# Optimization experiments

Hardware: AMD Instinct MI355X
Metric: run time of the kernel (lower is better)

The kernel has to match this reference:

```python
import jax, jax.numpy as jnp
import numpy as np

N_CHARS = 50257
CHAR = 512
HID = 1024
LENGTH = 2048


def setup_inputs() -> dict:
    key = jax.random.key(0)
    ks = jax.random.split(key, 8)
    s = 1.0 / np.sqrt(HID)
    sh = 1.0 / np.sqrt(HID)
    return {
        "inputs": jax.random.normal(ks[0], (HID,), jnp.float32),
        "embed": (jax.random.normal(ks[1], (N_CHARS, CHAR), jnp.float32) * 0.02),
        "W_ih": jax.random.uniform(ks[2], (4 * HID, CHAR), jnp.float32, -s, s),
        "W_hh": jax.random.uniform(ks[3], (4 * HID, HID), jnp.float32, -s, s),
        "b_ih": jax.random.uniform(ks[4], (4 * HID,), jnp.float32, -s, s),
        "b_hh": jax.random.uniform(ks[5], (4 * HID,), jnp.float32, -s, s),
        "W_head": jax.random.uniform(ks[6], (N_CHARS, HID), jnp.float32, -sh, sh),
        "b_head": jax.random.uniform(ks[7], (N_CHARS,), jnp.float32, -sh, sh),
        "length": LENGTH,
        "start": 5,
    }


def _lstm_cell(x, h, c, W_ih, W_hh, b_ih, b_hh):
    # PyTorch gate order: i, f, g, o
    gates = W_ih @ x + b_ih + W_hh @ h + b_hh  # [4H]
    i, f, g, o = jnp.split(gates, 4)
    i = jax.nn.sigmoid(i)
    f = jax.nn.sigmoid(f)
    g = jnp.tanh(g)
    o = jax.nn.sigmoid(o)
    c = f * c + i * g
    h = o * jnp.tanh(c)
    return h, c


def reference(inputs, embed, W_ih, W_hh, b_ih, b_hh, W_head, b_head, length, start):
    h0 = inputs                       # latent used as initial hidden state
    c0 = jnp.zeros_like(inputs)
    x0 = embed[start]                 # [CHAR]

    def step(carry, _):
        h, c, x = carry
        h, c = _lstm_cell(x, h, c, W_ih, W_hh, b_ih, b_hh)
        logits = W_head @ h + b_head  # [N_CHARS]
        char = jnp.argmax(logits)
        x = embed[char]
        return (h, c, x), (char, logits)

    _, (chars, logits) = jax.lax.scan(step, (h0, c0, x0), None, length=length)
    return chars, logits
```

## Files before the change

### kernel.cpp

```cpp
#include <hip/hip_runtime.h>
#include <stdint.h>
#include <math.h>

#define HID   1024
#define CHARD 512
#define NC    50257
#define TLEN  2048
#define NBLK  256
#define NTHR  512
#define NGRP2 2048
#define GR    25
#define GRREG 6
#define GRLDS 19
#define NBH   1571
#define SQ    4064.0f
#define INVSQ (1.0f/4064.0f)
#define QERR  (0.5f/4064.0f)
#define CANDR 192
#define FLAGSTRIDE 16

typedef unsigned long long ull;
typedef unsigned char u8;
typedef float f32x4 __attribute__((ext_vector_type(4)));

__device__ __forceinline__ unsigned ford(float f) {
    unsigned b = __float_as_uint(f);
    return (b & 0x80000000u) ? ~b : (b | 0x80000000u);
}
__device__ __forceinline__ float unford(unsigned u) {
    return __uint_as_float((u & 0x80000000u) ? (u & 0x7FFFFFFFu) : ~u);
}
__device__ __forceinline__ ull packkv(float v, unsigned j) {
    return ((ull)ford(v) << 32) | (ull)(0xFFFFFFFFu - j);
}
__device__ __forceinline__ unsigned ceil16(float v) {
    unsigned u = ford(v);
    return (u >> 16) + ((u & 0xFFFFu) ? 1u : 0u);
}
__device__ __forceinline__ ull umaxu(ull a, ull b) { return a > b ? a : b; }
__device__ __forceinline__ ull shflx_ull(ull v, int m) {
    unsigned lo = (unsigned)v, hi = (unsigned)(v >> 32);
    lo = __shfl_xor(lo, m);
    hi = __shfl_xor(hi, m);
    return ((ull)hi << 32) | lo;
}

#define ALOADF(p)    __hip_atomic_load((p), __ATOMIC_RELAXED, __HIP_MEMORY_SCOPE_AGENT)
#define ASTORE(p, v) __hip_atomic_store((p), (v), __ATOMIC_RELAXED, __HIP_MEMORY_SCOPE_AGENT)

__global__ __launch_bounds__(256) void k_init(const float* __restrict__ inputs,
                                              float* __restrict__ hh,
                                              float* __restrict__ c,
                                              unsigned* __restrict__ flagarea,
                                              unsigned* __restrict__ bm4,
                                              unsigned* __restrict__ abuf16)
{
    int g = blockIdx.x * 256 + threadIdx.x;
    if (g < HID) { hh[g] = inputs[g]; c[g] = 0.f; }
    for (int i = g; i < 2 * NBLK * FLAGSTRIDE; i += 2048) flagarea[i] = 0u;
    if (g < NGRP2) bm4[g] = 0u;
    for (int i = g; i < NC; i += 2048) abuf16[i] = 0u;
}

__global__ __launch_bounds__(256) void k_quant(const float* __restrict__ W,
                                               u8* __restrict__ W8)
{
    size_t base = ((size_t)blockIdx.x * 256 + threadIdx.x) * 16;
    if (base >= (size_t)NC * HID) return;
    const float4* src = (const float4*)(W + base);
    uint out[4];
    #pragma unroll
    for (int g = 0; g < 4; ++g) {
        float4 w = src[g];
        int a0 = (__float2int_rn(w.x * SQ) + 128) & 255;
        int a1 = (__float2int_rn(w.y * SQ) + 128) & 255;
        int a2 = (__float2int_rn(w.z * SQ) + 128) & 255;
        int a3 = (__float2int_rn(w.w * SQ) + 128) & 255;
        out[g] = (uint)(a0 | (a1 << 8) | (a2 << 16) | (a3 << 24));
    }
    *(uint4*)(W8 + base) = make_uint4(out[0], out[1], out[2], out[3]);
}

__device__ __forceinline__ float exact_logit(const float4* hs4,
                                             const float* __restrict__ W_head,
                                             const float* __restrict__ b_head,
                                             int j, int lane)
{
    const float4* wr = (const float4*)(W_head + (size_t)j * HID);
    float a = 0.f;
    #pragma unroll
    for (int m = 0; m < 4; ++m) {
        float4 w = wr[m * 64 + lane], v = hs4[m * 64 + lane];
        a = fmaf(w.x, v.x, a); a = fmaf(w.y, v.y, a);
        a = fmaf(w.z, v.z, a); a = fmaf(w.w, v.w, a);
    }
    #pragma unroll
    for (int off = 32; off > 0; off >>= 1) a += __shfl_xor(a, off);
    return a + b_head[j];
}

__device__ unsigned resolve_slim(const float4* hs4,
                                 const unsigned* bm4, const unsigned* abuf16,
                                 const float* __restrict__ W_head,
                                 const float* __restrict__ b_head,
                                 float Sh, unsigned gen16, int tid)
{
    __shared__ int s_cnt, s_gcnt;
    __shared__ int s_grps[32];
    __shared__ int s_rows[CANDR];
    __shared__ unsigned mred[8];
    __shared__ ull red8[8];

    const int wave = tid >> 6;
    const int lane = tid & 63;

    unsigned bv[4];
    unsigned m16 = 0u;
    #pragma unroll
    for (int k = 0; k < 4; ++k) {
        bv[k] = ALOADF(&bm4[tid * 4 + k]);
        if ((bv[k] & 0xFFFFu) == gen16) {
            unsigned v = bv[k] >> 16;
            if (v > m16) m16 = v;
        }
    }
    if (tid == 0) { s_cnt = 0; s_gcnt = 0; }
    #pragma unroll
    for (int off = 32; off > 0; off >>= 1) {
        unsigned o = __shfl_xor(m16, off);
        if (o > m16) m16 = o;
    }
    if (lane == 0) mred[wave] = m16;
    __syncthreads();
    m16 = mred[0];
    #pragma unroll
    for (int w = 1; w < 8; ++w) if (mred[w] > m16) m16 = mred[w];

    const float mtil_f = unford((m16 > 0 ? m16 - 1 : 0) << 16);
    const float E = QERR * Sh * 1.02f + 1e-4f;
    const float thresh = mtil_f - 2.0f * E;
    const unsigned th16 = ford(thresh) >> 16;

    #pragma unroll
    for (int k = 0; k < 4; ++k) {
        unsigned v = bv[k];
        if ((v & 0xFFFFu) == gen16 && (v >> 16) >= th16) {
            int p = atomicAdd(&s_gcnt, 1);
            if (p < 32) s_grps[p] = tid * 4 + k;
        }
    }
    __syncthreads();
    const int ngr = s_gcnt;
    int ncr;
    if (ngr <= 32) {
        for (int gq = wave; gq < ngr; gq += 8) {
            if (lane < GR) {
                const int j = s_grps[gq] * GR + lane;
                if (j < NC) {
                    unsigned a = ALOADF(&abuf16[j]);
                    if ((a & 0xFFFFu) == gen16 && (a >> 16) >= th16) {
                        int p = atomicAdd(&s_cnt, 1);
                        if (p < CANDR) s_rows[p] = j;
                    }
                }
            }
        }
        __syncthreads();
        ncr = s_cnt;
    } else ncr = CANDR + 1;

    ull best = 0ull;
    if (ncr <= CANDR) {
        for (int q = wave; q < ncr; q += 8) {
            const int j = s_rows[q];
            best = umaxu(best, packkv(exact_logit(hs4, W_head, b_head, j, lane),
                                      (unsigned)j));
        }
    } else {
        for (int i = wave; i < NGRP2; i += 8) {
            unsigned v = ALOADF(&bm4[i]);
            if ((v & 0xFFFFu) == gen16 && (v >> 16) >= th16) {
                const int j0 = i * GR;
                bool c = false;
                if (lane < GR && j0 + lane < NC) {
                    unsigned a = ALOADF(&abuf16[j0 + lane]);
                    c = ((a & 0xFFFFu) == gen16 && (a >> 16) >= th16);
                }
                ull cnd = __ballot(c);
                while (cnd) {
                    const int s = __builtin_ctzll(cnd);
                    cnd &= cnd - 1;
                    const int j = j0 + s;
                    best = umaxu(best, packkv(exact_logit(hs4, W_head, b_head, j, lane),
                                              (unsigned)j));
                }
            }
        }
    }
    __syncthreads();
    if (lane == 0) red8[wave] = best;
    __syncthreads();
    best = red8[0];
    #pragma unroll
    for (int w = 1; w < 8; ++w) best = umaxu(best, red8[w]);
    unsigned idx = 0xFFFFFFFFu - (unsigned)(best & 0xFFFFFFFFull);
    return idx < NC ? idx : (NC - 1);
}

__device__ __forceinline__ float dot16u(uint4 q, float4 h0, float4 h1,
                                        float4 h2, float4 h3)
{
    float a = 0.f;
    a = fmaf((float)(q.x & 255u), h0.x, a);
    a = fmaf((float)((q.x >> 8) & 255u), h0.y, a);
    a = fmaf((float)((q.x >> 16) & 255u), h0.z, a);
    a = fmaf((float)(q.x >> 24), h0.w, a);
    a = fmaf((float)(q.y & 255u), h1.x, a);
    a = fmaf((float)((q.y >> 8) & 255u), h1.y, a);
    a = fmaf((float)((q.y >> 16) & 255u), h1.z, a);
    a = fmaf((float)(q.y >> 24), h1.w, a);
    a = fmaf((float)(q.z & 255u), h2.x, a);
    a = fmaf((float)((q.z >> 8) & 255u), h2.y, a);
    a = fmaf((float)((q.z >> 16) & 255u), h2.z, a);
    a = fmaf((float)(q.z >> 24), h2.w, a);
    a = fmaf((float)(q.w & 255u), h3.x, a);
    a = fmaf((float)((q.w >> 8) & 255u), h3.y, a);
    a = fmaf((float)((q.w >> 16) & 255u), h3.z, a);
    a = fmaf((float)(q.w >> 24), h3.w, a);
    return a;
}

__global__ __launch_bounds__(NTHR, 1) void k_persist(
    const float* __restrict__ W_ih, const float* __restrict__ W_hh,
    const float* __restrict__ b_ih, const float* __restrict__ b_hh,
    const float* __restrict__ embed,
    const float* __restrict__ W_head, const float* __restrict__ b_head,
    const u8* __restrict__ W8,
    float* hh, unsigned* abuf16, unsigned* bm4,
    float* __restrict__ chars_out, const int* __restrict__ startp,
    unsigned* flags, unsigned* gen)
{
    __shared__ uint4  w8L[8][GRLDS][64];
    __shared__ float4 hs4[HID / 4];
    __shared__ float4 xs4[CHARD / 4];
    __shared__ float  sred[8], sred2[8];

    const int b    = blockIdx.x;
    const int tid  = threadIdx.x;
    const int wave = tid >> 6;
    const int lane = tid & 63;
    const int rL   = b * 4 + wave;
    const int g    = b * 8 + wave;
    const int jb   = g * GR;
    const u8* Wp   = W8 + (size_t)jb * HID;

    uint4 qb[GRREG];
    #pragma unroll
    for (int rr = 0; rr < GRREG; ++rr) {
        const int j = jb + rr;
        qb[rr] = (j < NC) ? ((const uint4*)(Wp + (size_t)rr * HID))[lane]
                          : make_uint4(0, 0, 0, 0);
    }
    #pragma unroll
    for (int rr = 0; rr < GRLDS; ++rr) {
        const int j = jb + GRREG + rr;
        w8L[wave][rr][lane] = (j < NC)
            ? ((const uint4*)(Wp + (size_t)(GRREG + rr) * HID))[lane]
            : make_uint4(0, 0, 0, 0);
    }

    float bsum[4] = {0.f, 0.f, 0.f, 0.f};
    if (wave < 4) {
        #pragma unroll
        for (int q = 0; q < 4; ++q) bsum[q] = b_ih[q * HID + rL] + b_hh[q * HID + rL];
    }
    float creg = 0.f;
    __syncthreads();

    float Sh;
    {
        float sa = 0.f;
        if (tid < 256) {
            float4 hv = ((const float4*)hh)[tid];
            hs4[tid] = hv;
            sa = fabsf(hv.x) + fabsf(hv.y) + fabsf(hv.z) + fabsf(hv.w);
        }
        #pragma unroll
        for (int off = 32; off > 0; off >>= 1) sa += __shfl_xor(sa, off);
        if (lane == 0) sred[wave] = sa;
        __syncthreads();
        Sh = 0.f;
        #pragma unroll
        for (int w = 0; w < 8; ++w) Sh += sred[w];
    }

    unsigned bk = 0;

    #define GRIDBAR()                                                              \
    do {                                                                           \
        ++bk;                                                                      \
        __syncthreads();                                                           \
        if (b == 0) {                                                              \
            if (tid > 0 && tid < NBLK) {                                           \
                int guard = 0;                                                     \
                while (ALOADF(&flags[tid * FLAGSTRIDE]) < bk) {                    \
                    __builtin_amdgcn_s_sleep(1);                                   \
                    if (++guard > (1 << 24)) break;                                \
                }                                                                  \
            }                                                                      \
            __syncthreads();                                                       \
            if (tid < NBLK)                                                        \
                ASTORE(&gen[tid * FLAGSTRIDE], bk);                                \
        } else {                                                                   \
            if (tid == 0) {                                                        \
                ASTORE(&flags[b * FLAGSTRIDE], bk);                                \
                int guard = 0;                                                     \
                while (ALOADF(&gen[b * FLAGSTRIDE]) < bk) {                        \
                    __builtin_amdgcn_s_sleep(1);                                   \
                    if (++guard > (1 << 24)) break;                                \
                }                                                                  \
            }                                                                      \
            __syncthreads();                                                       \
        }                                                                          \
    } while (0)

    for (int t = 0; t < TLEN; ++t) {
        unsigned idx;
        if (t == 0) {
            idx = (unsigned)startp[0];
        } else {
            idx = resolve_slim(hs4, bm4, abuf16, W_head, b_head, Sh,
                               (unsigned)t & 0xFFFFu, tid);
            if (b == 0 && tid == 0) chars_out[t - 1] = (float)idx;
        }
        if (tid < 128) xs4[tid] = ((const float4*)(embed + (size_t)idx * CHARD))[tid];
        __syncthreads();

        if (wave < 4) {
            float acc[4];
            #pragma unroll
            for (int q = 0; q < 4; ++q) {
                const float4* wi = (const float4*)(W_ih + (size_t)(q * HID + rL) * CHARD);
                const float4* wh = (const float4*)(W_hh + (size_t)(q * HID + rL) * HID);
                float a = 0.f;
                #pragma unroll
                for (int m = 0; m < 2; ++m) {
                    float4 w = wi[m * 64 + lane], v = xs4[m * 64 + lane];
                    a = fmaf(w.x, v.x, a); a = fmaf(w.y, v.y, a);
                    a = fmaf(w.z, v.z, a); a = fmaf(w.w, v.w, a);
                }
                #pragma unroll
                for (int m = 0; m < 4; ++m) {
                    float4 w = wh[m * 64 + lane], v = hs4[m * 64 + lane];
                    a = fmaf(w.x, v.x, a); a = fmaf(w.y, v.y, a);
                    a = fmaf(w.z, v.z, a); a = fmaf(w.w, v.w, a);
                }
                acc[q] = a;
            }
            #pragma unroll
            for (int q = 0; q < 4; ++q) {
                #pragma unroll
                for (int off = 32; off > 0; off >>= 1) acc[q] += __shfl_xor(acc[q], off);
            }
            if (lane == 0) {
                float ig = 1.f / (1.f + expf(-(acc[0] + bsum[0])));
                float fg = 1.f / (1.f + expf(-(acc[1] + bsum[1])));
                float gg = tanhf(acc[2] + bsum[2]);
                float og = 1.f / (1.f + expf(-(acc[3] + bsum[3])));
                creg = fg * creg + ig * gg;
                ASTORE(&hh[(size_t)(t + 1) * HID + rL], og * tanhf(creg));
            }
        }

        GRIDBAR();

        {
            float sa = 0.f, ss = 0.f;
            if (tid < 256) {
                float4 hv = ((const float4*)(hh + (size_t)(t + 1) * HID))[tid];
                hs4[tid] = hv;
                sa = fabsf(hv.x) + fabsf(hv.y) + fabsf(hv.z) + fabsf(hv.w);
                ss = hv.x + hv.y + hv.z + hv.w;
            }
            #pragma unroll
            for (int off = 32; off > 0; off >>= 1) {
                sa += __shfl_xor(sa, off);
                ss += __shfl_xor(ss, off);
            }
            if (lane == 0) { sred[wave] = sa; sred2[wave] = ss; }
        }
        __syncthreads();
        float Hsum = 0.f;
        Sh = 0.f;
        #pragma unroll
        for (int w = 0; w < 8; ++w) { Sh += sred[w]; Hsum += sred2[w]; }

        const float4 H0 = hs4[lane * 4 + 0];
        const float4 H1 = hs4[lane * 4 + 1];
        const float4 H2 = hs4[lane * 4 + 2];
        const float4 H3 = hs4[lane * 4 + 3];
        const unsigned genN = (unsigned)(t + 1) & 0xFFFFu;

        if (jb < NC) {
            ull pmw = 0ull;
            float sv = -3.0e38f;
            #pragma unroll
            for (int rr = 0; rr < GRREG; ++rr) {
                const int j = jb + rr;
                if (j < NC) {
                    float a = dot16u(qb[rr], H0, H1, H2, H3);
                    #pragma unroll
                    for (int off = 32; off > 0; off >>= 1) a += __shfl_xor(a, off);
                    const float v = (a - 128.f * Hsum) * INVSQ + b_head[j];
                    if (lane == rr) sv = v;
                    pmw = umaxu(pmw, packkv(v, (unsigned)j));
                }
            }
            #pragma unroll
            for (int rr = 0; rr < GRLDS; ++rr) {
                const int j = jb + GRREG + rr;
                if (j < NC) {
                    float a = dot16u(w8L[wave][rr][lane], H0, H1, H2, H3);
                    #pragma unroll
                    for (int off = 32; off > 0; off >>= 1) a += __shfl_xor(a, off);
                    const float v = (a - 128.f * Hsum) * INVSQ + b_head[j];
                    if (lane == GRREG + rr) sv = v;
                    pmw = umaxu(pmw, packkv(v, (unsigned)j));
                }
            }
            const float gtop = unford((unsigned)(pmw >> 32));
            const float E2 = QERR * Sh * 1.02f + 1e-4f;
            if (lane < GR && (jb + lane) < NC && sv >= gtop - 2.0f * E2)
                ASTORE(&abuf16[jb + lane], (ceil16(sv) << 16) | genN);
            if (lane == 0)
                ASTORE(&bm4[g], (ceil16(gtop) << 16) | genN);
        }

        GRIDBAR();
    }

    if (b == 0) {
        unsigned idx = resolve_slim(hs4, bm4, abuf16, W_head, b_head, Sh,
                                    (unsigned)TLEN & 0xFFFFu, tid);
        if (tid == 0) chars_out[TLEN - 1] = (float)idx;
    }
    #undef GRIDBAR
}

#define GJ 64
#define GT 128
#define GK 16
__global__ __launch_bounds__(256) void k_gemm(const float* __restrict__ W_head,
                                              const float* __restrict__ b_head,
                                              const float* __restrict__ hh,
                                              float* __restrict__ logits)
{
    __shared__ float Ws[GK][GJ + 4];
    __shared__ float Hs[GK][GT + 1];

    const int tid = threadIdx.x;
    const int j0 = blockIdx.x * GJ;
    const int t0 = blockIdx.y * GT;
    const int tj = tid & 15;
    const int tt = tid >> 4;

    const int wlj = tid >> 2;
    const int wlk = (tid & 3) * 4;
    const int hlt = tid >> 1;
    const int hlk = (tid & 1) * 8;
    const float* Wrow = W_head + (size_t)(j0 + wlj) * HID;
    const bool wvalid = (j0 + wlj) < NC;

    float acc[8][4];
    #pragma unroll
    for (int bb = 0; bb < 8; ++bb)
        #pragma unroll
        for (int a = 0; a < 4; ++a) acc[bb][a] = 0.f;

    for (int k0 = 0; k0 < HID; k0 += GK) {
        __syncthreads();
        float4 wv = wvalid ? *(const float4*)(Wrow + k0 + wlk) : make_float4(0, 0, 0, 0);
        Ws[wlk + 0][wlj] = wv.x; Ws[wlk + 1][wlj] = wv.y;
        Ws[wlk + 2][wlj] = wv.z; Ws[wlk + 3][wlj] = wv.w;
        const float* hp = hh + (size_t)(t0 + hlt + 1) * HID + k0 + hlk;
        float4 a0 = *(const float4*)hp;
        float4 a1 = *(const float4*)(hp + 4);
        Hs[hlk + 0][hlt] = a0.x; Hs[hlk + 1][hlt] = a0.y;
        Hs[hlk + 2][hlt] = a0.z; Hs[hlk + 3][hlt] = a0.w;
        Hs[hlk + 4][hlt] = a1.x; Hs[hlk + 5][hlt] = a1.y;
        Hs[hlk + 6][hlt] = a1.z; Hs[hlk + 7][hlt] = a1.w;
        __syncthreads();
        #pragma unroll
        for (int kk = 0; kk < GK; ++kk) {
            float4 w4 = *(const float4*)&Ws[kk][tj * 4];
            float hvv[8];
            #pragma unroll
            for (int bb = 0; bb < 8; ++bb) hvv[bb] = Hs[kk][tt + 16 * bb];
            #pragma unroll
            for (int bb = 0; bb < 8; ++bb) {
                acc[bb][0] = fmaf(w4.x, hvv[bb], acc[bb][0]);
                acc[bb][1] = fmaf(w4.y, hvv[bb], acc[bb][1]);
                acc[bb][2] = fmaf(w4.z, hvv[bb], acc[bb][2]);
                acc[bb][3] = fmaf(w4.w, hvv[bb], acc[bb][3]);
            }
        }
    }

    const int j = j0 + tj * 4;
    float b0 = (j + 0 < NC) ? b_head[j + 0] : 0.f;
    float b1 = (j + 1 < NC) ? b_head[j + 1] : 0.f;
    float b2 = (j + 2 < NC) ? b_head[j + 2] : 0.f;
    float b3 = (j + 3 < NC) ? b_head[j + 3] : 0.f;
    #pragma unroll
    for (int bb = 0; bb < 8; ++bb) {
        const int t = t0 + tt + 16 * bb;
        float* dst = logits + (size_t)t * NC + j;
        if (j + 3 < NC) {
            f32x4 o = { acc[bb][0] + b0, acc[bb][1] + b1,
                        acc[bb][2] + b2, acc[bb][3] + b3 };
            __builtin_nontemporal_store(o, (f32x4*)dst);
        } else {
            if (j + 0 < NC) dst[0] = acc[bb][0] + b0;
            if (j + 1 < NC) dst[1] = acc[bb][1] + b1;
            if (j + 2 < NC) dst[2] = acc[bb][2] + b2;
        }
    }
}

__global__ __launch_bounds__(256) void k_init_fb(const float* __restrict__ inputs,
                                                 const int* __restrict__ startp,
                                                 float* __restrict__ h0,
                                                 float* __restrict__ c,
                                                 ull* __restrict__ blockmax)
{
    int tid = blockIdx.x * 256 + threadIdx.x;
    if (tid < NBH) blockmax[tid] = (tid == 0) ? packkv(3.0e38f, (unsigned)startp[0]) : 0ull;
    if (tid < HID) { h0[tid] = inputs[tid]; c[tid] = 0.f; }
}

__global__ __launch_bounds__(256) void k_lstm_fb(const float* __restrict__ W_ih,
                                                 const float* __restrict__ W_hh,
                                                 const float* __restrict__ b_ih,
                                                 const float* __restrict__ b_hh,
                                                 const float* __restrict__ embed,
                                                 const ull* __restrict__ blockmax,
                                                 const float* __restrict__ h_in,
                                                 float* __restrict__ h_out,
                                                 float* __restrict__ c,
                                                 float* __restrict__ chars_out,
                                                 int t)
{
    __shared__ float4 xs4[CHARD / 4];
    __shared__ float4 hs4[HID / 4];
    __shared__ ull    red[256];
    const int tid = threadIdx.x;
    ull pm = 0ull;
    for (int i = tid; i < NBH; i += 256) pm = umaxu(pm, blockmax[i]);
    red[tid] = pm;
    __syncthreads();
    for (int s = 128; s > 0; s >>= 1) {
        if (tid < s) red[tid] = umaxu(red[tid], red[tid + s]);
        __syncthreads();
    }
    const unsigned idx = 0xFFFFFFFFu - (unsigned)(red[0] & 0xFFFFFFFFull);
    if (t > 0 && blockIdx.x == 0 && tid == 0) chars_out[t - 1] = (float)idx;
    const float4* ex = (const float4*)(embed + (size_t)idx * CHARD);
    if (tid < 128) xs4[tid] = ex[tid];
    hs4[tid] = ((const float4*)h_in)[tid];
    __syncthreads();
    const int wave = tid >> 6, lane = tid & 63;
    const int r = blockIdx.x * 4 + wave;
    float acc[4];
    #pragma unroll
    for (int q = 0; q < 4; ++q) {
        const float4* wi = (const float4*)(W_ih + (size_t)(q * HID + r) * CHARD);
        const float4* wh = (const float4*)(W_hh + (size_t)(q * HID + r) * HID);
        float a = 0.f;
        #pragma unroll
        for (int m = 0; m < 2; ++m) {
            float4 w = wi[m * 64 + lane], v = xs4[m * 64 + lane];
            a = fmaf(w.x, v.x, a); a = fmaf(w.y, v.y, a);
            a = fmaf(w.z, v.z, a); a = fmaf(w.w, v.w, a);
        }
        #pragma unroll
        for (int m = 0; m < 4; ++m) {
            float4 w = wh[m * 64 + lane], v = hs4[m * 64 + lane];
            a = fmaf(w.x, v.x, a); a = fmaf(w.y, v.y, a);
            a = fmaf(w.z, v.z, a); a = fmaf(w.w, v.w, a);
        }
        acc[q] = a;
    }
    #pragma unroll
    for (int q = 0; q < 4; ++q)
        #pragma unroll
        for (int off = 32; off > 0; off >>= 1) acc[q] += __shfl_xor(acc[q], off);
    if (lane == 0) {
        float zi = acc[0] + b_ih[r]           + b_hh[r];
        float zf = acc[1] + b_ih[HID + r]     + b_hh[HID + r];
        float zg = acc[2] + b_ih[2 * HID + r] + b_hh[2 * HID + r];
        float zo = acc[3] + b_ih[3 * HID + r] + b_hh[3 * HID + r];
        float ig = 1.f / (1.f + expf(-zi));
        float fg = 1.f / (1.f + expf(-zf));
        float gg = tanhf(zg);
        float og = 1.f / (1.f + expf(-zo));
        float cn = fg * c[r] + ig * gg;
        c[r] = cn;
        h_out[r] = og * tanhf(cn);
    }
}

__global__ __launch_bounds__(256) void k_head_fb(const float* __restrict__ W_head,
                                                 const float* __restrict__ b_head,
                                                 const float* __restrict__ h_in,
                                                 float* __restrict__ logits,
                                                 ull* __restrict__ blockmax)
{
    __shared__ float4 hs4[HID / 4];
    __shared__ ull    wmax[4];
    const int tid = threadIdx.x;
    hs4[tid] = ((const float4*)h_in)[tid];
    __syncthreads();
    const int wave = tid >> 6, lane = tid & 63;
    const int base = blockIdx.x * 32 + wave * 8;
    ull pm = 0ull;
    #pragma unroll
    for (int rep = 0; rep < 8; ++rep) {
        const int j = base + rep;
        if (j < NC) {
            const float4* w = (const float4*)(W_head + (size_t)j * HID);
            float a = 0.f;
            #pragma unroll
            for (int m = 0; m < 4; ++m) {
                float4 ww = w[m * 64 + lane], v = hs4[m * 64 + lane];
                a = fmaf(ww.x, v.x, a); a = fmaf(ww.y, v.y, a);
                a = fmaf(ww.z, v.z, a); a = fmaf(ww.w, v.w, a);
            }
            #pragma unroll
            for (int off = 32; off > 0; off >>= 1) a += __shfl_xor(a, off);
            const float v = a + b_head[j];
            if (lane == 0) __builtin_nontemporal_store(v, &logits[j]);
            pm = umaxu(pm, packkv(v, (unsigned)j));
        }
    }
    if (lane == 0) wmax[wave] = pm;
    __syncthreads();
    if (tid == 0)
        blockmax[blockIdx.x] = umaxu(umaxu(wmax[0], wmax[1]), umaxu(wmax[2], wmax[3]));
}

__global__ __launch_bounds__(256) void k_final_fb(const ull* __restrict__ blockmax,
                                                  float* __restrict__ chars_out)
{
    __shared__ ull red[256];
    const int tid = threadIdx.x;
    ull pm = 0ull;
    for (int i = tid; i < NBH; i += 256) pm = umaxu(pm, blockmax[i]);
    red[tid] = pm;
    __syncthreads();
    for (int s = 128; s > 0; s >>= 1) {
        if (tid < s) red[tid] = umaxu(red[tid], red[tid + s]);
        __syncthreads();
    }
    if (tid == 0)
        chars_out[TLEN - 1] = (float)(0xFFFFFFFFu - (unsigned)(red[0] & 0xFFFFFFFFull));
}

extern "C" void kernel_launch(void* const* d_in, const int* in_sizes, int n_in,
                              void* d_out, int out_size, void* d_ws, size_t ws_size,
                              hipStream_t stream)
{
    const float* inputs = (const float*)d_in[0];
    const float* embed  = (const float*)d_in[1];
    const float* W_ih   = (const float*)d_in[2];
    const float* W_hh   = (const float*)d_in[3];
    const float* b_ih   = (const float*)d_in[4];
    const float* b_hh   = (const float*)d_in[5];
    const float* W_head = (const float*)d_in[6];
    const float* b_head = (const float*)d_in[7];
    const int*   startp = (const int*)d_in[9];

    float* out        = (float*)d_out;
    float* chars_out  = out;
    float* logits_out = out + TLEN;

    char* ws = (char*)d_ws;
    const size_t off_hh  = 0;
    const size_t off_c   = off_hh + (size_t)(TLEN + 1) * HID * 4;
    const size_t off_ab  = (off_c + (size_t)HID * 4 + 15) & ~(size_t)15;
    const size_t off_bm  = (off_ab + (size_t)NC * 4 + 15) & ~(size_t)15;
    const size_t off_fl  = (off_bm + (size_t)NGRP2 * 4 + 63) & ~(size_t)63;
    const size_t off_w8  = (off_fl + (size_t)(2 * NBLK * FLAGSTRIDE) * 4 + 15)
                           & ~(size_t)15;
    const size_t need    = off_w8 + (size_t)NC * HID;

    if (ws_size >= need) {
        float*    hh     = (float*)(ws + off_hh);
        float*    c      = (float*)(ws + off_c);
        unsigned* abuf16 = (unsigned*)(ws + off_ab);
        unsigned* bm4    = (unsigned*)(ws + off_bm);
        unsigned* flags  = (unsigned*)(ws + off_fl);
        unsigned* gen    = flags + NBLK * FLAGSTRIDE;
        u8*       W8     = (u8*)(ws + off_w8);

        hipLaunchKernelGGL(k_init, dim3(8), dim3(256), 0, stream,
                           inputs, hh, c, flags, bm4, abuf16);
        hipLaunchKernelGGL(k_quant, dim3((NC * HID / 16 + 255) / 256), dim3(256), 0,
                           stream, W_head, W8);
        hipLaunchKernelGGL(k_persist, dim3(NBLK), dim3(NTHR), 0, stream,
                           W_ih, W_hh, b_ih, b_hh, embed, W_head, b_head, W8,
                           hh, abuf16, bm4, chars_out, startp, flags, gen);
        hipLaunchKernelGGL(k_gemm, dim3((NC + GJ - 1) / GJ, TLEN / GT), dim3(256), 0,
                           stream, W_head, b_head, hh, logits_out);
    } else {
        float* h0 = (float*)(ws);
        float* h1 = (float*)(ws + 4096);
        float* c  = (float*)(ws + 8192);
        ull* blockmax = (ull*)(ws + 12288);
        hipLaunchKernelGGL(k_init_fb, dim3(7), dim3(256), 0, stream,
                           inputs, startp, h0, c, blockmax);
        for (int t = 0; t < TLEN; ++t) {
            const float* hin = (t & 1) ? h1 : h0;
            float*       hout = (t & 1) ? h0 : h1;
            hipLaunchKernelGGL(k_lstm_fb, dim3(256), dim3(256), 0, stream,
                               W_ih, W_hh, b_ih, b_hh, embed, blockmax,
                               hin, hout, c, chars_out, t);
            hipLaunchKernelGGL(k_head_fb, dim3(NBH), dim3(256), 0, stream,
                               W_head, b_head, hout,
                               logits_out + (size_t)t * NC, blockmax);
        }
        hipLaunchKernelGGL(k_final_fb, dim3(1), dim3(256), 0, stream, blockmax, chars_out);
    }
}
```

Measured before the change: 45.43 ms.

## Replace second grid barrier with generation-tagged polling of per-group max records

Drops the grid-wide barrier after the head scoring phase. Each group now publishes a 64-bit record holding its top score, the top row index and the second-best score, tagged with the step number. The resolver polls these records until every one carries the current tag. Because the record names the top row directly, candidate rows can be taken from it without scanning the per-row buffer. This halves the barriers per timestep, at the cost of spin-polling and relying on the ordering of relaxed atomics plus an explicit waitcnt for correctness.

```diff
diff --git a/kernel.cpp b/kernel.cpp
--- a/kernel.cpp
+++ b/kernel.cpp
@@ -35,15 +35,10 @@
 }
 __device__ __forceinline__ unsigned ceil16(float v) {
     unsigned u = ford(v);
-    return (u >> 16) + ((u & 0xFFFFu) ? 1u : 0u);
+    unsigned r = (u >> 16) + ((u & 0xFFFFu) ? 1u : 0u);
+    return r > 0xFFFFu ? 0xFFFFu : r;
 }
 __device__ __forceinline__ ull umaxu(ull a, ull b) { return a > b ? a : b; }
-__device__ __forceinline__ ull shflx_ull(ull v, int m) {
-    unsigned lo = (unsigned)v, hi = (unsigned)(v >> 32);
-    lo = __shfl_xor(lo, m);
-    hi = __shfl_xor(hi, m);
-    return ((ull)hi << 32) | lo;
-}
 
 #define ALOADF(p)    __hip_atomic_load((p), __ATOMIC_RELAXED, __HIP_MEMORY_SCOPE_AGENT)
 #define ASTORE(p, v) __hip_atomic_store((p), (v), __ATOMIC_RELAXED, __HIP_MEMORY_SCOPE_AGENT)
@@ -52,13 +47,13 @@
                                               float* __restrict__ hh,
                                               float* __restrict__ c,
                                               unsigned* __restrict__ flagarea,
-                                              unsigned* __restrict__ bm4,
+                                              ull* __restrict__ bm8,
                                               unsigned* __restrict__ abuf16)
 {
     int g = blockIdx.x * 256 + threadIdx.x;
     if (g < HID) { hh[g] = inputs[g]; c[g] = 0.f; }
     for (int i = g; i < 2 * NBLK * FLAGSTRIDE; i += 2048) flagarea[i] = 0u;
-    if (g < NGRP2) bm4[g] = 0u;
+    if (g < NGRP2) bm8[g] = 0ull;
     for (int i = g; i < NC; i += 2048) abuf16[i] = 0u;
 }
 
@@ -99,8 +94,8 @@
     return a + b_head[j];
 }
 
-__device__ unsigned resolve_slim(const float4* hs4,
-                                 const unsigned* bm4, const unsigned* abuf16,
+__device__ unsigned resolve_poll(const float4* hs4,
+                                 const ull* bm8, const unsigned* abuf16,
                                  const float* __restrict__ W_head,
                                  const float* __restrict__ b_head,
                                  float Sh, unsigned gen16, int tid)
@@ -108,51 +103,69 @@
     __shared__ int s_cnt, s_gcnt;
     __shared__ int s_grps[32];
     __shared__ int s_rows[CANDR];
-    __shared__ unsigned mred[8];
+    __shared__ unsigned mred[4];
     __shared__ ull red8[8];
 
     const int wave = tid >> 6;
     const int lane = tid & 63;
 
-    unsigned bv[4];
+    ull rec[8];
     unsigned m16 = 0u;
-    #pragma unroll
-    for (int k = 0; k < 4; ++k) {
-        bv[k] = ALOADF(&bm4[tid * 4 + k]);
-        if ((bv[k] & 0xFFFFu) == gen16) {
-            unsigned v = bv[k] >> 16;
-            if (v > m16) m16 = v;
-        }
-    }
     if (tid == 0) { s_cnt = 0; s_gcnt = 0; }
-    #pragma unroll
-    for (int off = 32; off > 0; off >>= 1) {
-        unsigned o = __shfl_xor(m16, off);
-        if (o > m16) m16 = o;
-    }
-    if (lane == 0) mred[wave] = m16;
+    if (wave < 4) {
+        const int base = tid * 8;
+        int guard = 0;
+        for (;;) {
+            bool ok = true;
+            #pragma unroll
+            for (int k = 0; k < 8; ++k) {
+                rec[k] = ALOADF(&bm8[base + k]);
+                ok = ok && (((unsigned)rec[k] & 0xFFFFu) == gen16);
+            }
+            if (ok) break;
+            __builtin_amdgcn_s_sleep(1);
+            if (++guard > (1 << 22)) break;
+        }
+        #pragma unroll
+        for (int k = 0; k < 8; ++k) {
+            unsigned t16 = (unsigned)(rec[k] >> 48);
+            if (t16 > m16) m16 = t16;
+        }
+        #pragma unroll
+        for (int off = 32; off > 0; off >>= 1) {
+            unsigned o = __shfl_xor(m16, off);
+            if (o > m16) m16 = o;
+        }
+        if (lane == 0) mred[wave] = m16;
+    }
     __syncthreads();
     m16 = mred[0];
     #pragma unroll
-    for (int w = 1; w < 8; ++w) if (mred[w] > m16) m16 = mred[w];
+    for (int w = 1; w < 4; ++w) if (mred[w] > m16) m16 = mred[w];
 
     const float mtil_f = unford((m16 > 0 ? m16 - 1 : 0) << 16);
     const float E = QERR * Sh * 1.02f + 1e-4f;
     const float thresh = mtil_f - 2.0f * E;
     const unsigned th16 = ford(thresh) >> 16;
 
-    #pragma unroll
-    for (int k = 0; k < 4; ++k) {
-        unsigned v = bv[k];
-        if ((v & 0xFFFFu) == gen16 && (v >> 16) >= th16) {
-            int p = atomicAdd(&s_gcnt, 1);
-            if (p < 32) s_grps[p] = tid * 4 + k;
+    if (wave < 4) {
+        #pragma unroll
+        for (int k = 0; k < 8; ++k) {
+            unsigned t16 = (unsigned)(rec[k] >> 48);
+            unsigned s16 = (unsigned)(rec[k] >> 16) & 0xFFFFu;
+            if (t16 >= th16) {
+                int p = atomicAdd(&s_cnt, 1);
+                if (p < CANDR) s_rows[p] = (int)((rec[k] >> 32) & 0xFFFFu);
+            }
+            if (s16 >= th16) {
+                int p = atomicAdd(&s_gcnt, 1);
+                if (p < 32) s_grps[p] = tid * 8 + k;
+            }
         }
     }
     __syncthreads();
     const int ngr = s_gcnt;
-    int ncr;
-    if (ngr <= 32) {
+    if (ngr > 0 && ngr <= 32) {
         for (int gq = wave; gq < ngr; gq += 8) {
             if (lane < GR) {
                 const int j = s_grps[gq] * GR + lane;
@@ -165,9 +178,9 @@
                 }
             }
         }
-        __syncthreads();
-        ncr = s_cnt;
-    } else ncr = CANDR + 1;
+    }
+    __syncthreads();
+    const int ncr = (ngr <= 32) ? s_cnt : (CANDR + 1);
 
     ull best = 0ull;
     if (ncr <= CANDR) {
@@ -178,21 +191,25 @@
         }
     } else {
         for (int i = wave; i < NGRP2; i += 8) {
-            unsigned v = ALOADF(&bm4[i]);
-            if ((v & 0xFFFFu) == gen16 && (v >> 16) >= th16) {
-                const int j0 = i * GR;
-                bool c = false;
-                if (lane < GR && j0 + lane < NC) {
-                    unsigned a = ALOADF(&abuf16[j0 + lane]);
-                    c = ((a & 0xFFFFu) == gen16 && (a >> 16) >= th16);
-                }
-                ull cnd = __ballot(c);
-                while (cnd) {
-                    const int s = __builtin_ctzll(cnd);
-                    cnd &= cnd - 1;
-                    const int j = j0 + s;
-                    best = umaxu(best, packkv(exact_logit(hs4, W_head, b_head, j, lane),
-                                              (unsigned)j));
+            ull rv = ALOADF(&bm8[i]);
+            if (((unsigned)rv & 0xFFFFu) == gen16) {
+                unsigned t16 = (unsigned)(rv >> 48);
+                unsigned s16 = (unsigned)(rv >> 16) & 0xFFFFu;
+                if (t16 >= th16 || s16 >= th16) {
+                    const int j0 = i * GR;
+                    bool c = false;
+                    if (lane < GR && j0 + lane < NC) {
+                        unsigned a = ALOADF(&abuf16[j0 + lane]);
+                        c = ((a & 0xFFFFu) == gen16 && (a >> 16) >= th16);
+                    }
+                    ull cnd = __ballot(c);
+                    while (cnd) {
+                        const int s = __builtin_ctzll(cnd);
+                        cnd &= cnd - 1;
+                        const int j = j0 + s;
+                        best = umaxu(best, packkv(exact_logit(hs4, W_head, b_head, j, lane),
+                                                  (unsigned)j));
+                    }
                 }
             }
         }
@@ -236,9 +253,9 @@
     const float* __restrict__ embed,
     const float* __restrict__ W_head, const float* __restrict__ b_head,
     const u8* __restrict__ W8,
-    float* hh, unsigned* abuf16, unsigned* bm4,
+    float* hh, unsigned* abuf16, ull* bm8,
     float* __restrict__ chars_out, const int* __restrict__ startp,
-    unsigned* flags, unsigned* gen)
+    unsigned* flags, unsigned* rel)
 {
     __shared__ uint4  w8L[8][GRLDS][64];
     __shared__ float4 hs4[HID / 4];
@@ -294,42 +311,12 @@
         for (int w = 0; w < 8; ++w) Sh += sred[w];
     }
 
-    unsigned bk = 0;
-
-    #define GRIDBAR()                                                              \
-    do {                                                                           \
-        ++bk;                                                                      \
-        __syncthreads();                                                           \
-        if (b == 0) {                                                              \
-            if (tid > 0 && tid < NBLK) {                                           \
-                int guard = 0;                                                     \
-                while (ALOADF(&flags[tid * FLAGSTRIDE]) < bk) {                    \
-                    __builtin_amdgcn_s_sleep(1);                                   \
-                    if (++guard > (1 << 24)) break;                                \
-                }                                                                  \
-            }                                                                      \
-            __syncthreads();                                                       \
-            if (tid < NBLK)                                                        \
-                ASTORE(&gen[tid * FLAGSTRIDE], bk);                                \
-        } else {                                                                   \
-            if (tid == 0) {                                                        \
-                ASTORE(&flags[b * FLAGSTRIDE], bk);                                \
-                int guard = 0;                                                     \
-                while (ALOADF(&gen[b * FLAGSTRIDE]) < bk) {                        \
-                    __builtin_amdgcn_s_sleep(1);                                   \
-                    if (++guard > (1 << 24)) break;                                \
-                }                                                                  \
-            }                                                                      \
-            __syncthreads();                                                       \
-        }                                                                          \
-    } while (0)
-
     for (int t = 0; t < TLEN; ++t) {
         unsigned idx;
         if (t == 0) {
             idx = (unsigned)startp[0];
         } else {
-            idx = resolve_slim(hs4, bm4, abuf16, W_head, b_head, Sh,
+            idx = resolve_poll(hs4, bm8, abuf16, W_head, b_head, Sh,
                                (unsigned)t & 0xFFFFu, tid);
             if (b == 0 && tid == 0) chars_out[t - 1] = (float)idx;
         }
@@ -372,7 +359,32 @@
             }
         }
 
-        GRIDBAR();
+        {
+            const unsigned bka = (unsigned)(t + 1);
+            __syncthreads();
+            if (b == 0) {
+                if (tid > 0 && tid < NBLK) {
+                    int guard = 0;
+                    while (ALOADF(&flags[tid * FLAGSTRIDE]) < bka) {
+                        __builtin_amdgcn_s_sleep(1);
+                        if (++guard > (1 << 24)) break;
+                    }
+                }
+                __syncthreads();
+                if (tid < NBLK)
+                    ASTORE(&rel[tid * FLAGSTRIDE], bka);
+            } else {
+                if (tid == 0) {
+                    ASTORE(&flags[b * FLAGSTRIDE], bka);
+                    int guard = 0;
+                    while (ALOADF(&rel[b * FLAGSTRIDE]) < bka) {
+                        __builtin_amdgcn_s_sleep(1);
+                        if (++guard > (1 << 24)) break;
+                    }
+                }
+                __syncthreads();
+            }
+        }
 
         {
             float sa = 0.f, ss = 0.f;
@@ -401,6 +413,7 @@
         const float4 H3 = hs4[lane * 4 + 3];
         const unsigned genN = (unsigned)(t + 1) & 0xFFFFu;
 
+        ull recv = (ull)genN;
         if (jb < NC) {
             ull pmw = 0ull;
             float sv = -3.0e38f;
@@ -428,23 +441,27 @@
                     pmw = umaxu(pmw, packkv(v, (unsigned)j));
                 }
             }
+            const unsigned grow = 0xFFFFFFFFu - (unsigned)(pmw & 0xFFFFFFFFull);
             const float gtop = unford((unsigned)(pmw >> 32));
+            const int stop = (int)grow - jb;
+            float s2 = (lane == stop) ? -3.0e38f : sv;
+            #pragma unroll
+            for (int off = 32; off > 0; off >>= 1) s2 = fmaxf(s2, __shfl_xor(s2, off));
             const float E2 = QERR * Sh * 1.02f + 1e-4f;
             if (lane < GR && (jb + lane) < NC && sv >= gtop - 2.0f * E2)
                 ASTORE(&abuf16[jb + lane], (ceil16(sv) << 16) | genN);
-            if (lane == 0)
-                ASTORE(&bm4[g], (ceil16(gtop) << 16) | genN);
-        }
-
-        GRIDBAR();
+            recv = ((ull)ceil16(gtop) << 48) | ((ull)(grow & 0xFFFFu) << 32)
+                 | ((ull)ceil16(s2) << 16) | (ull)genN;
+        }
+        asm volatile("s_waitcnt vmcnt(0)" ::: "memory");
+        if (lane == 0) ASTORE(&bm8[g], recv);
     }
 
     if (b == 0) {
-        unsigned idx = resolve_slim(hs4, bm4, abuf16, W_head, b_head, Sh,
+        unsigned idx = resolve_poll(hs4, bm8, abuf16, W_head, b_head, Sh,
                                     (unsigned)TLEN & 0xFFFFu, tid);
         if (tid == 0) chars_out[TLEN - 1] = (float)idx;
     }
-    #undef GRIDBAR
 }
 
 #define GJ 64
@@ -527,6 +544,8 @@
     }
 }
 
+__device__ __forceinline__ ull packkv_fb(float v, unsigned j) { return packkv(v, j); }
+
 __global__ __launch_bounds__(256) void k_init_fb(const float* __restrict__ inputs,
                                                  const int* __restrict__ startp,
                                                  float* __restrict__ h0,
@@ -534,7 +553,7 @@
                                                  ull* __restrict__ blockmax)
 {
     int tid = blockIdx.x * 256 + threadIdx.x;
-    if (tid < NBH) blockmax[tid] = (tid == 0) ? packkv(3.0e38f, (unsigned)startp[0]) : 0ull;
+    if (tid < NBH) blockmax[tid] = (tid == 0) ? packkv_fb(3.0e38f, (unsigned)startp[0]) : 0ull;
     if (tid < HID) { h0[tid] = inputs[tid]; c[tid] = 0.f; }
 }
 
@@ -687,8 +706,8 @@
     const size_t off_hh  = 0;
     const size_t off_c   = off_hh + (size_t)(TLEN + 1) * HID * 4;
     const size_t off_ab  = (off_c + (size_t)HID * 4 + 15) & ~(size_t)15;
-    const size_t off_bm  = (off_ab + (size_t)NC * 4 + 15) & ~(size_t)15;
-    const size_t off_fl  = (off_bm + (size_t)NGRP2 * 4 + 63) & ~(size_t)63;
+    const size_t off_bm  = (off_ab + (size_t)NC * 4 + 63) & ~(size_t)63;
+    const size_t off_fl  = (off_bm + (size_t)NGRP2 * 8 + 63) & ~(size_t)63;
     const size_t off_w8  = (off_fl + (size_t)(2 * NBLK * FLAGSTRIDE) * 4 + 15)
                            & ~(size_t)15;
     const size_t need    = off_w8 + (size_t)NC * HID;
@@ -697,18 +716,18 @@
         float*    hh     = (float*)(ws + off_hh);
         float*    c      = (float*)(ws + off_c);
         unsigned* abuf16 = (unsigned*)(ws + off_ab);
-        unsigned* bm4    = (unsigned*)(ws + off_bm);
+        ull*      bm8    = (ull*)(ws + off_bm);
         unsigned* flags  = (unsigned*)(ws + off_fl);
-        unsigned* gen    = flags + NBLK * FLAGSTRIDE;
+        unsigned* rel    = flags + NBLK * FLAGSTRIDE;
         u8*       W8     = (u8*)(ws + off_w8);
 
         hipLaunchKernelGGL(k_init, dim3(8), dim3(256), 0, stream,
-                           inputs, hh, c, flags, bm4, abuf16);
+                           inputs, hh, c, flags, bm8, abuf16);
         hipLaunchKernelGGL(k_quant, dim3((NC * HID / 16 + 255) / 256), dim3(256), 0,
                            stream, W_head, W8);
         hipLaunchKernelGGL(k_persist, dim3(NBLK), dim3(NTHR), 0, stream,
                            W_ih, W_hh, b_ih, b_hh, embed, W_head, b_head, W8,
-                           hh, abuf16, bm4, chars_out, startp, flags, gen);
+                           hh, abuf16, bm8, chars_out, startp, flags, rel);
         hipLaunchKernelGGL(k_gemm, dim3((NC + GJ - 1) / GJ, TLEN / GT), dim3(256), 0,
                            stream, W_head, b_head, hh, logits_out);
     } else {
```

After: 79.59 ms. 1.75x slower.
